# Kernel optimization log

Hardware: AMD Instinct MI355X
Metric: run time of the kernel (lower is better)

## Reference

```python
import jax, jax.numpy as jnp
import numpy as np
from jax import lax

B, L, E, H, V = 256, 1024, 128, 256, 64


def setup_inputs() -> dict:
    key = jax.random.key(0)
    ks = jax.random.split(key, 8)
    x = jax.random.randint(ks[0], (B, L), 0, V, dtype=jnp.int64)
    hidden = jnp.zeros((B, H), dtype=jnp.float32)
    embedding = jax.random.normal(ks[1], (V, E), dtype=jnp.float32)
    W_e = jax.random.normal(ks[2], (H, E), dtype=jnp.float32) * 0.01
    b_e = jnp.zeros((H,), dtype=jnp.float32)
    W_h = jax.random.normal(ks[3], (H, H), dtype=jnp.float32) * 0.01
    b_h = jnp.zeros((H,), dtype=jnp.float32)
    fc_w = jax.random.normal(ks[4], (V, H), dtype=jnp.float32) * (1.0 / np.sqrt(H))
    fc_b = jax.random.normal(ks[5], (V,), dtype=jnp.float32) * 0.01
    return {"x": x, "hidden": hidden, "embedding": embedding, "W_e": W_e,
            "b_e": b_e, "W_h": W_h, "b_h": b_h, "fc_w": fc_w, "fc_b": fc_b}


def reference(x, hidden, embedding, W_e, b_e, W_h, b_h, fc_w, fc_b):
    # x: [B, L] int ids -> embed: [B, L, E]
    x_embed = embedding[x]
    # Precompute the input projection for all timesteps (parallel GEMM):
    # x_embed @ W_e.T + b_e  -> [B, L, H]
    x_proj = jnp.einsum('ble,he->blh', x_embed, W_e) + b_e
    x_proj_t = jnp.swapaxes(x_proj, 0, 1)  # [L, B, H]

    def step(h_prev, xp_t):
        # h_t = tanh(x_t W_e^T + b_e + h_{t-1} W_h^T + b_h)
        h_t = jnp.tanh(xp_t + h_prev @ W_h.T + b_h)
        return h_t, h_t

    final_hidden, outs = lax.scan(step, hidden, x_proj_t)  # outs: [L, B, H]
    output = jnp.swapaxes(outs, 0, 1)  # [B, L, H]
    logits = jnp.einsum('blh,vh->blv', output, fc_w) + fc_b  # [B, L, V]
    return logits, final_hidden
```

## Files before the change

### kernel.cpp

```cpp
#include <hip/hip_runtime.h>
#include <hip/hip_bf16.h>

#define BB 256
#define LL 1024
#define EE 128
#define HH 256
#define VV 64

typedef short bf16x8 __attribute__((ext_vector_type(8)));
typedef float f32x4 __attribute__((ext_vector_type(4)));


__device__ __forceinline__ unsigned short f2bf(float v) {
    __hip_bfloat16 h = __float2bfloat16(v);
    return *reinterpret_cast<unsigned short*>(&h);
}
__device__ __forceinline__ float bf2f(unsigned short u) {
    __hip_bfloat16 h = *reinterpret_cast<__hip_bfloat16*>(&u);
    return __bfloat162float(h);
}

__global__ void prep_kernel(const float* __restrict__ emb,
                            const float* __restrict__ W_e,
                            const float* __restrict__ b_e,
                            const float* __restrict__ W_h,
                            const float* __restrict__ b_h,
                            const float* __restrict__ fc_w,
                            float* __restrict__ ws) {
    int t = blockIdx.x * 256 + threadIdx.x;
    if (t < 16384) {
        int v = t >> 8, j = t & 255;
        float s = b_e[j] + b_h[j];
        const float* ev = emb + v * EE;
        const float* wr = W_e + j * EE;
#pragma unroll 8
        for (int e = 0; e < EE; ++e) s = fmaf(ev[e], wr[e], s);
        ws[t] = s;
    } else if (t < 24576) {
        int q = t - 16384;
        int f = q >> 6, l = q & 63;
        int nt = f >> 3, kt = f & 7;
        int row = 16 * nt + (l & 15);
        int k0 = 32 * kt + 8 * (l >> 4);
        unsigned short* p = (unsigned short*)((char*)ws + 65536 + f * 1024 + l * 16);
#pragma unroll
        for (int i = 0; i < 8; ++i) p[i] = f2bf(W_h[row * HH + k0 + i]);
    } else {
        int q = t - 24576;
        int f = q >> 6, l = q & 63;
        int nt = f >> 3, kt = f & 7;
        int row = 16 * nt + (l & 15);
        int k0 = 32 * kt + 8 * (l >> 4);
        unsigned short* ph = (unsigned short*)((char*)ws + 196608 + f * 1024 + l * 16);
        unsigned short* pl = (unsigned short*)((char*)ws + 229376 + f * 1024 + l * 16);
#pragma unroll
        for (int i = 0; i < 8; ++i) {
            float v = fc_w[row * HH + k0 + i];
            unsigned short hi = f2bf(v);
            float res = v - bf2f(hi);
            ph[i] = hi;
            pl[i] = f2bf(res);
        }
    }
}

__device__ __forceinline__ float tanh_fast(float x) {
    float a = fabsf(x);
    float e = __expf(-2.0f * a);
    float r = (1.0f - e) * __builtin_amdgcn_rcpf(1.0f + e);
    return copysignf(r, x);
}

__launch_bounds__(384, 1)
__global__ void rnn_kernel(const int* __restrict__ x,
                           const float* __restrict__ hidden,
                           const float* __restrict__ fc_b,
                           const float* __restrict__ ws,
                           float* __restrict__ out) {
    __shared__ __align__(16) unsigned short hb[2][HH];

    const int tid = threadIdx.x;
    const int b = blockIdx.x;
    const int w = tid >> 6;
    const int l = tid & 63;

    const char* wsB  = (const char*)ws + 65536;
    const char* wsFH = (const char*)ws + 196608;
    const char* wsFL = (const char*)ws + 229376;
    const float* table = ws;

    float* outL = out;
    float* outH = out + (size_t)BB * LL * VV;

    if (tid < HH) hb[0][tid] = f2bf(hidden[b * HH + tid]);

    if (w < 4) {
        bf16x8 Bf[4][8];
#pragma unroll
        for (int nt2 = 0; nt2 < 4; ++nt2)
#pragma unroll
            for (int kt = 0; kt < 8; ++kt)
                Bf[nt2][kt] = *(const bf16x8*)(wsB + (((4 * w + nt2) * 8 + kt) * 1024) + l * 16);

        bf16x8 a[8];
        bf16x8 zz = {0, 0, 0, 0, 0, 0, 0, 0};
#pragma unroll
        for (int kt = 0; kt < 8; ++kt) a[kt] = zz;

        float xp[4];
        int xv_nn;
        {
            int xv0 = x[b * LL];
#pragma unroll
            for (int nt2 = 0; nt2 < 4; ++nt2)
                xp[nt2] = table[xv0 * HH + 16 * (4 * w + nt2) + (l & 15)];
            xv_nn = x[b * LL + 1];
        }
        const int abyte = (l >> 4) * 16;

        __syncthreads();
#pragma unroll 1
        for (int u = 0; u <= LL; ++u) {
            if (u < LL) {
                const char* hcur = (const char*)hb[u & 1];
                if ((l & 15) == 0) {
#pragma unroll
                    for (int kt = 0; kt < 8; ++kt)
                        a[kt] = *(const bf16x8*)(hcur + kt * 64 + abyte);
                }
                float xpn[4];
                if (u < LL - 1) {
#pragma unroll
                    for (int nt2 = 0; nt2 < 4; ++nt2)
                        xpn[nt2] = table[xv_nn * HH + 16 * (4 * w + nt2) + (l & 15)];
                }
                int xv3 = (u < LL - 2) ? x[b * LL + u + 2] : 0;

                f32x4 acc[4];
#pragma unroll
                for (int nt2 = 0; nt2 < 4; ++nt2)
                    acc[nt2] = (f32x4){xp[nt2], xp[nt2], xp[nt2], xp[nt2]};
#pragma unroll
                for (int kt = 0; kt < 8; ++kt)
#pragma unroll
                    for (int nt2 = 0; nt2 < 4; ++nt2)
                        acc[nt2] = __builtin_amdgcn_mfma_f32_16x16x32_bf16(
                            a[kt], Bf[nt2][kt], acc[nt2], 0, 0, 0);

                unsigned short* hnxt = hb[(u + 1) & 1];
#pragma unroll
                for (int nt2 = 0; nt2 < 4; ++nt2) {
                    float hval = tanh_fast(acc[nt2][0]);
                    if (l < 16) {
                        hnxt[16 * (4 * w + nt2) + l] = f2bf(hval);
                        if (u == LL - 1)
                            outH[b * HH + 16 * (4 * w + nt2) + l] = hval;
                    }
                }
#pragma unroll
                for (int nt2 = 0; nt2 < 4; ++nt2) xp[nt2] = xpn[nt2];
                xv_nn = xv3;
            }
            __syncthreads();
        }
    } else {
        const int nb = (w - 4) * 2;
        bf16x8 FH[2][8], FL[2][8];
#pragma unroll
        for (int nt2 = 0; nt2 < 2; ++nt2)
#pragma unroll
            for (int kt = 0; kt < 8; ++kt) {
                FH[nt2][kt] = *(const bf16x8*)(wsFH + (((nb + nt2) * 8 + kt) * 1024) + l * 16);
                FL[nt2][kt] = *(const bf16x8*)(wsFL + (((nb + nt2) * 8 + kt) * 1024) + l * 16);
            }
        float fcb[2];
#pragma unroll
        for (int nt2 = 0; nt2 < 2; ++nt2)
            fcb[nt2] = fc_b[16 * (nb + nt2) + (l & 15)];

        bf16x8 a[8];
        bf16x8 zz = {0, 0, 0, 0, 0, 0, 0, 0};
#pragma unroll
        for (int kt = 0; kt < 8; ++kt) a[kt] = zz;
        const int abyte = (l >> 4) * 16;

        __syncthreads();
#pragma unroll 1
        for (int u = 0; u <= LL; ++u) {
            if (u >= 1) {
                const char* hcur = (const char*)hb[u & 1];
                if ((l & 15) == 0) {
#pragma unroll
                    for (int kt = 0; kt < 8; ++kt)
                        a[kt] = *(const bf16x8*)(hcur + kt * 64 + abyte);
                }
                f32x4 aH[2], aL[2];
#pragma unroll
                for (int nt2 = 0; nt2 < 2; ++nt2) {
                    aH[nt2] = (f32x4){fcb[nt2], fcb[nt2], fcb[nt2], fcb[nt2]};
                    aL[nt2] = (f32x4){0.f, 0.f, 0.f, 0.f};
                }
#pragma unroll
                for (int kt = 0; kt < 8; ++kt)
#pragma unroll
                    for (int nt2 = 0; nt2 < 2; ++nt2) {
                        aH[nt2] = __builtin_amdgcn_mfma_f32_16x16x32_bf16(
                            a[kt], FH[nt2][kt], aH[nt2], 0, 0, 0);
                        aL[nt2] = __builtin_amdgcn_mfma_f32_16x16x32_bf16(
                            a[kt], FL[nt2][kt], aL[nt2], 0, 0, 0);
                    }
                if (l < 16) {
                    const int s = u - 1;
#pragma unroll
                    for (int nt2 = 0; nt2 < 2; ++nt2)
                        outL[((size_t)b * LL + s) * VV + 16 * (nb + nt2) + (l & 15)] =
                            aH[nt2][0] + aL[nt2][0];
                }
            }
            __syncthreads();
        }
    }
}

extern "C" void kernel_launch(void* const* d_in, const int* in_sizes, int n_in,
                              void* d_out, int out_size, void* d_ws, size_t ws_size,
                              hipStream_t stream) {
    const int*   x      = (const int*)  d_in[0];
    const float* hidden = (const float*)d_in[1];
    const float* emb    = (const float*)d_in[2];
    const float* W_e    = (const float*)d_in[3];
    const float* b_e    = (const float*)d_in[4];
    const float* W_h    = (const float*)d_in[5];
    const float* b_h    = (const float*)d_in[6];
    const float* fc_w   = (const float*)d_in[7];
    const float* fc_b   = (const float*)d_in[8];
    float* out = (float*)d_out;
    float* ws  = (float*)d_ws;

    prep_kernel<<<104, 256, 0, stream>>>(emb, W_e, b_e, W_h, b_h, fc_w, ws);
    rnn_kernel<<<BB, 384, 0, stream>>>(x, hidden, fc_b, ws, out);
}
```

Measured before the change: 791.6 us.

## Merge recurrence and output-projection waves, split MFMA accumulator chains, batch logit stores

Drops the two dedicated fc waves. Each of the four remaining waves now computes its 16-column slice of the logits for the previous step alongside its recurrence slice, and the block shrinks to 256 threads. The recurrence MFMA chain is split into four independent accumulators per tile to shorten dependent latency. Logits are buffered in registers for 8 steps and stored in batches, and the prep kernel's dot product is vectorised. In exchange, each wave holds more weights in registers and the critical per-step path gains the fc MFMAs.

```diff
diff --git a/kernel.cpp b/kernel.cpp
--- a/kernel.cpp
+++ b/kernel.cpp
@@ -9,6 +9,7 @@
 
 typedef short bf16x8 __attribute__((ext_vector_type(8)));
 typedef float f32x4 __attribute__((ext_vector_type(4)));
+typedef float v4f  __attribute__((ext_vector_type(4)));
 
 
 __device__ __forceinline__ unsigned short f2bf(float v) {
@@ -31,10 +32,13 @@
     if (t < 16384) {
         int v = t >> 8, j = t & 255;
         float s = b_e[j] + b_h[j];
-        const float* ev = emb + v * EE;
-        const float* wr = W_e + j * EE;
-#pragma unroll 8
-        for (int e = 0; e < EE; ++e) s = fmaf(ev[e], wr[e], s);
+        const v4f* ev = (const v4f*)(emb + v * EE);
+        const v4f* wr = (const v4f*)(W_e + j * EE);
+#pragma unroll
+        for (int e = 0; e < EE / 4; ++e) {
+            v4f a = ev[e], c = wr[e];
+            s += a.x * c.x + a.y * c.y + a.z * c.z + a.w * c.w;
+        }
         ws[t] = s;
     } else if (t < 24576) {
         int q = t - 16384;
@@ -71,7 +75,7 @@
     return copysignf(r, x);
 }
 
-__launch_bounds__(384, 1)
+__launch_bounds__(256, 1)
 __global__ void rnn_kernel(const int* __restrict__ x,
                            const float* __restrict__ hidden,
                            const float* __restrict__ fc_b,
@@ -89,135 +93,146 @@
     const char* wsFL = (const char*)ws + 229376;
     const float* table = ws;
 
-    float* outL = out;
     float* outH = out + (size_t)BB * LL * VV;
 
+    bf16x8 Bf[4][8];
+#pragma unroll
+    for (int n = 0; n < 4; ++n)
+#pragma unroll
+        for (int k = 0; k < 8; ++k)
+            Bf[n][k] = *(const bf16x8*)(wsB + (((4 * w + n) * 8 + k) * 1024) + l * 16);
+    bf16x8 FH[8], FL[8];
+#pragma unroll
+    for (int k = 0; k < 8; ++k) {
+        FH[k] = *(const bf16x8*)(wsFH + ((w * 8 + k) * 1024) + l * 16);
+        FL[k] = *(const bf16x8*)(wsFL + ((w * 8 + k) * 1024) + l * 16);
+    }
+    const float fcb = fc_b[16 * w + (l & 15)];
+
+    bf16x8 a[8];
+    bf16x8 zz = {0, 0, 0, 0, 0, 0, 0, 0};
+#pragma unroll
+    for (int k = 0; k < 8; ++k) a[k] = zz;
+    const int abyte = (l >> 4) * 16;
+
     if (tid < HH) hb[0][tid] = f2bf(hidden[b * HH + tid]);
 
-    if (w < 4) {
-        bf16x8 Bf[4][8];
-#pragma unroll
-        for (int nt2 = 0; nt2 < 4; ++nt2)
-#pragma unroll
-            for (int kt = 0; kt < 8; ++kt)
-                Bf[nt2][kt] = *(const bf16x8*)(wsB + (((4 * w + nt2) * 8 + kt) * 1024) + l * 16);
-
-        bf16x8 a[8];
-        bf16x8 zz = {0, 0, 0, 0, 0, 0, 0, 0};
-#pragma unroll
-        for (int kt = 0; kt < 8; ++kt) a[kt] = zz;
-
-        float xp[4];
-        int xv_nn;
-        {
-            int xv0 = x[b * LL];
-#pragma unroll
-            for (int nt2 = 0; nt2 < 4; ++nt2)
-                xp[nt2] = table[xv0 * HH + 16 * (4 * w + nt2) + (l & 15)];
-            xv_nn = x[b * LL + 1];
-        }
-        const int abyte = (l >> 4) * 16;
-
-        __syncthreads();
+    const int xoff = l & 15;
+    float xp[4];
+    int xv_next;
+    {
+        int xv0 = x[b * LL];
+#pragma unroll
+        for (int n = 0; n < 4; ++n)
+            xp[n] = table[xv0 * HH + 16 * (4 * w + n) + xoff];
+        xv_next = x[b * LL + 1];
+    }
+    float lb[8];
+    float* outLbase = out + (size_t)b * LL * VV + 16 * w + (l & 15);
+
+    __syncthreads();
+
 #pragma unroll 1
-        for (int u = 0; u <= LL; ++u) {
-            if (u < LL) {
-                const char* hcur = (const char*)hb[u & 1];
-                if ((l & 15) == 0) {
-#pragma unroll
-                    for (int kt = 0; kt < 8; ++kt)
-                        a[kt] = *(const bf16x8*)(hcur + kt * 64 + abyte);
-                }
-                float xpn[4];
-                if (u < LL - 1) {
-#pragma unroll
-                    for (int nt2 = 0; nt2 < 4; ++nt2)
-                        xpn[nt2] = table[xv_nn * HH + 16 * (4 * w + nt2) + (l & 15)];
-                }
-                int xv3 = (u < LL - 2) ? x[b * LL + u + 2] : 0;
-
-                f32x4 acc[4];
-#pragma unroll
-                for (int nt2 = 0; nt2 < 4; ++nt2)
-                    acc[nt2] = (f32x4){xp[nt2], xp[nt2], xp[nt2], xp[nt2]};
-#pragma unroll
-                for (int kt = 0; kt < 8; ++kt)
-#pragma unroll
-                    for (int nt2 = 0; nt2 < 4; ++nt2)
-                        acc[nt2] = __builtin_amdgcn_mfma_f32_16x16x32_bf16(
-                            a[kt], Bf[nt2][kt], acc[nt2], 0, 0, 0);
-
-                unsigned short* hnxt = hb[(u + 1) & 1];
-#pragma unroll
-                for (int nt2 = 0; nt2 < 4; ++nt2) {
-                    float hval = tanh_fast(acc[nt2][0]);
-                    if (l < 16) {
-                        hnxt[16 * (4 * w + nt2) + l] = f2bf(hval);
-                        if (u == LL - 1)
-                            outH[b * HH + 16 * (4 * w + nt2) + l] = hval;
-                    }
-                }
-#pragma unroll
-                for (int nt2 = 0; nt2 < 4; ++nt2) xp[nt2] = xpn[nt2];
-                xv_nn = xv3;
-            }
+    for (int tb = 0; tb < LL; tb += 8) {
+#pragma unroll
+        for (int u = 0; u < 8; ++u) {
+            const int t = tb + u;
+            const char* hcur = (const char*)hb[u & 1];
+            if ((l & 15) == 0) {
+#pragma unroll
+                for (int k = 0; k < 8; ++k)
+                    a[k] = *(const bf16x8*)(hcur + k * 64 + abyte);
+            }
+            float xpn[4];
+            int xv3 = 0;
+            if (t + 1 < LL) {
+#pragma unroll
+                for (int n = 0; n < 4; ++n)
+                    xpn[n] = table[xv_next * HH + 16 * (4 * w + n) + xoff];
+                xv3 = (t + 2 < LL) ? x[b * LL + t + 2] : 0;
+            } else {
+#pragma unroll
+                for (int n = 0; n < 4; ++n) xpn[n] = 0.f;
+            }
+
+            {
+                f32x4 g0 = (f32x4){fcb, fcb, fcb, fcb};
+                f32x4 g1 = (f32x4){0.f, 0.f, 0.f, 0.f};
+                f32x4 r0 = (f32x4){0.f, 0.f, 0.f, 0.f};
+                f32x4 r1 = (f32x4){0.f, 0.f, 0.f, 0.f};
+#pragma unroll
+                for (int k = 0; k < 4; ++k) {
+                    g0 = __builtin_amdgcn_mfma_f32_16x16x32_bf16(a[k], FH[k], g0, 0, 0, 0);
+                    g1 = __builtin_amdgcn_mfma_f32_16x16x32_bf16(a[4 + k], FH[4 + k], g1, 0, 0, 0);
+                    r0 = __builtin_amdgcn_mfma_f32_16x16x32_bf16(a[k], FL[k], r0, 0, 0, 0);
+                    r1 = __builtin_amdgcn_mfma_f32_16x16x32_bf16(a[4 + k], FL[4 + k], r1, 0, 0, 0);
+                }
+                lb[(u + 7) & 7] = (g0[0] + g1[0]) + (r0[0] + r1[0]);
+            }
+
+            f32x4 c[4][4];
+#pragma unroll
+            for (int n = 0; n < 4; ++n) {
+                c[n][0] = (f32x4){xp[n], xp[n], xp[n], xp[n]};
+                c[n][1] = (f32x4){0.f, 0.f, 0.f, 0.f};
+                c[n][2] = (f32x4){0.f, 0.f, 0.f, 0.f};
+                c[n][3] = (f32x4){0.f, 0.f, 0.f, 0.f};
+#pragma unroll
+                for (int q = 0; q < 4; ++q) {
+                    c[n][q] = __builtin_amdgcn_mfma_f32_16x16x32_bf16(a[2 * q], Bf[n][2 * q], c[n][q], 0, 0, 0);
+                    c[n][q] = __builtin_amdgcn_mfma_f32_16x16x32_bf16(a[2 * q + 1], Bf[n][2 * q + 1], c[n][q], 0, 0, 0);
+                }
+            }
+
+            if (u == 0) {
+                if (tb > 0 && l < 16) {
+#pragma unroll
+                    for (int k2 = 0; k2 < 8; ++k2)
+                        outLbase[(size_t)(tb - 8 + k2) * VV] = lb[k2];
+                }
+            }
+
+            unsigned short* hnxt = hb[(u + 1) & 1];
+#pragma unroll
+            for (int n = 0; n < 4; ++n) {
+                float s = (c[n][0][0] + c[n][1][0]) + (c[n][2][0] + c[n][3][0]);
+                float hval = tanh_fast(s);
+                if (l < 16) {
+                    hnxt[16 * (4 * w + n) + l] = f2bf(hval);
+                    if (u == 7 && tb == LL - 8)
+                        outH[b * HH + 16 * (4 * w + n) + l] = hval;
+                }
+            }
+#pragma unroll
+            for (int n = 0; n < 4; ++n) xp[n] = xpn[n];
+            xv_next = xv3;
             __syncthreads();
         }
-    } else {
-        const int nb = (w - 4) * 2;
-        bf16x8 FH[2][8], FL[2][8];
-#pragma unroll
-        for (int nt2 = 0; nt2 < 2; ++nt2)
-#pragma unroll
-            for (int kt = 0; kt < 8; ++kt) {
-                FH[nt2][kt] = *(const bf16x8*)(wsFH + (((nb + nt2) * 8 + kt) * 1024) + l * 16);
-                FL[nt2][kt] = *(const bf16x8*)(wsFL + (((nb + nt2) * 8 + kt) * 1024) + l * 16);
-            }
-        float fcb[2];
-#pragma unroll
-        for (int nt2 = 0; nt2 < 2; ++nt2)
-            fcb[nt2] = fc_b[16 * (nb + nt2) + (l & 15)];
-
-        bf16x8 a[8];
-        bf16x8 zz = {0, 0, 0, 0, 0, 0, 0, 0};
-#pragma unroll
-        for (int kt = 0; kt < 8; ++kt) a[kt] = zz;
-        const int abyte = (l >> 4) * 16;
-
-        __syncthreads();
-#pragma unroll 1
-        for (int u = 0; u <= LL; ++u) {
-            if (u >= 1) {
-                const char* hcur = (const char*)hb[u & 1];
-                if ((l & 15) == 0) {
-#pragma unroll
-                    for (int kt = 0; kt < 8; ++kt)
-                        a[kt] = *(const bf16x8*)(hcur + kt * 64 + abyte);
-                }
-                f32x4 aH[2], aL[2];
-#pragma unroll
-                for (int nt2 = 0; nt2 < 2; ++nt2) {
-                    aH[nt2] = (f32x4){fcb[nt2], fcb[nt2], fcb[nt2], fcb[nt2]};
-                    aL[nt2] = (f32x4){0.f, 0.f, 0.f, 0.f};
-                }
-#pragma unroll
-                for (int kt = 0; kt < 8; ++kt)
-#pragma unroll
-                    for (int nt2 = 0; nt2 < 2; ++nt2) {
-                        aH[nt2] = __builtin_amdgcn_mfma_f32_16x16x32_bf16(
-                            a[kt], FH[nt2][kt], aH[nt2], 0, 0, 0);
-                        aL[nt2] = __builtin_amdgcn_mfma_f32_16x16x32_bf16(
-                            a[kt], FL[nt2][kt], aL[nt2], 0, 0, 0);
-                    }
-                if (l < 16) {
-                    const int s = u - 1;
-#pragma unroll
-                    for (int nt2 = 0; nt2 < 2; ++nt2)
-                        outL[((size_t)b * LL + s) * VV + 16 * (nb + nt2) + (l & 15)] =
-                            aH[nt2][0] + aL[nt2][0];
-                }
-            }
-            __syncthreads();
+    }
+
+    {
+        const char* hcur = (const char*)hb[0];
+        if ((l & 15) == 0) {
+#pragma unroll
+            for (int k = 0; k < 8; ++k)
+                a[k] = *(const bf16x8*)(hcur + k * 64 + abyte);
+        }
+        f32x4 g0 = (f32x4){fcb, fcb, fcb, fcb};
+        f32x4 g1 = (f32x4){0.f, 0.f, 0.f, 0.f};
+        f32x4 r0 = (f32x4){0.f, 0.f, 0.f, 0.f};
+        f32x4 r1 = (f32x4){0.f, 0.f, 0.f, 0.f};
+#pragma unroll
+        for (int k = 0; k < 4; ++k) {
+            g0 = __builtin_amdgcn_mfma_f32_16x16x32_bf16(a[k], FH[k], g0, 0, 0, 0);
+            g1 = __builtin_amdgcn_mfma_f32_16x16x32_bf16(a[4 + k], FH[4 + k], g1, 0, 0, 0);
+            r0 = __builtin_amdgcn_mfma_f32_16x16x32_bf16(a[k], FL[k], r0, 0, 0, 0);
+            r1 = __builtin_amdgcn_mfma_f32_16x16x32_bf16(a[4 + k], FL[4 + k], r1, 0, 0, 0);
+        }
+        lb[7] = (g0[0] + g1[0]) + (r0[0] + r1[0]);
+        if (l < 16) {
+#pragma unroll
+            for (int k2 = 0; k2 < 8; ++k2)
+                outLbase[(size_t)(LL - 8 + k2) * VV] = lb[k2];
         }
     }
 }
@@ -238,5 +253,5 @@
     float* ws  = (float*)d_ws;
 
     prep_kernel<<<104, 256, 0, stream>>>(emb, W_e, b_e, W_h, b_h, fc_w, ws);
-    rnn_kernel<<<BB, 384, 0, stream>>>(x, hidden, fc_b, ws, out);
-}
+    rnn_kernel<<<BB, 256, 0, stream>>>(x, hidden, fc_b, ws, out);
+}
```

New measurement: 996.5 us. 25.9% more time.
